# Optimization experiments

Hardware: AMD Instinct MI355X
Metric: run time of the kernel (lower is better)

The kernel has to match this reference:

```python
import jax, jax.numpy as jnp
import numpy as np

V, E, H, B, T, K = 50000, 100, 128, 128, 512, 12
HD = H // 2  # per-direction LSTM hidden = 64
START, STOP = 10, 11


def _lstm_params(k):
    k1, k2, k3, k4 = jax.random.split(k, 4)
    s = 1.0 / np.sqrt(HD)
    return (jax.random.uniform(k1, (4 * HD, E), minval=-s, maxval=s),
            jax.random.uniform(k2, (4 * HD, HD), minval=-s, maxval=s),
            jax.random.uniform(k3, (4 * HD,), minval=-s, maxval=s),
            jax.random.uniform(k4, (4 * HD,), minval=-s, maxval=s))


def setup_inputs() -> dict:
    key = jax.random.key(0)
    ks = jax.random.split(key, 10)
    sentences = jax.random.randint(ks[0], (B, T), 0, V)
    emb = jax.random.normal(ks[1], (V, E)) * 0.1
    Wih_f, Whh_f, bih_f, bhh_f = _lstm_params(ks[2])
    Wih_b, Whh_b, bih_b, bhh_b = _lstm_params(ks[3])
    W_out = jax.random.normal(ks[4], (K, H)) * 0.05
    b_out = jnp.zeros((K,), dtype=jnp.float32)
    transitions = jax.random.normal(ks[5], (K, K))
    transitions = transitions.at[:, START].set(-10000.0).at[STOP, :].set(-10000.0)
    h0 = jax.random.normal(ks[6], (2, B, HD))
    c0 = jax.random.normal(ks[7], (2, B, HD))
    return dict(sentences=sentences, emb=emb,
                Wih_f=Wih_f, Whh_f=Whh_f, bih_f=bih_f, bhh_f=bhh_f,
                Wih_b=Wih_b, Whh_b=Whh_b, bih_b=bih_b, bhh_b=bhh_b,
                W_out=W_out, b_out=b_out, transitions=transitions, h0=h0, c0=c0)


def _lstm_dir(x, h0, c0, Wih, Whh, bih, bhh):
    # x: [T,B,E]; PyTorch gate order i,f,g,o
    def step(carry, xt):
        h, c = carry
        g = xt @ Wih.T + h @ Whh.T + bih + bhh  # [B,4HD]
        i, f, gg, o = jnp.split(g, 4, axis=-1)
        c = jax.nn.sigmoid(f) * c + jax.nn.sigmoid(i) * jnp.tanh(gg)
        h = jax.nn.sigmoid(o) * jnp.tanh(c)
        return (h, c), h
    _, hs = jax.lax.scan(step, (h0, c0), x)
    return hs  # [T,B,HD]


def _viterbi(emis, trans):
    # emis: [T,K]
    def step(prev, em_t):
        v = prev[:, None] + trans          # [K_from, K_to]
        nxt = em_t + jnp.max(v, axis=0)
        return nxt, jnp.argmax(v, axis=0)  # backpointer per to-tag
    last, bps = jax.lax.scan(step, emis[0], emis[1:])  # bps: [T-1,K]
    last_tag = jnp.argmax(last)
    score = jnp.max(last)
    def back(tag, bp):
        prev = bp[tag]
        return prev, prev
    _, head = jax.lax.scan(back, last_tag, bps, reverse=True)  # tags[0..T-2]
    path = jnp.concatenate([head, last_tag[None]])
    return score, path


def reference(sentences, emb, Wih_f, Whh_f, bih_f, bhh_f,
              Wih_b, Whh_b, bih_b, bhh_b, W_out, b_out,
              transitions, h0, c0):
    x = emb[sentences]              # [B,T,E]
    xt = jnp.swapaxes(x, 0, 1)      # [T,B,E]
    hf = _lstm_dir(xt, h0[0], c0[0], Wih_f, Whh_f, bih_f, bhh_f)
    hb = _lstm_dir(xt[::-1], h0[1], c0[1], Wih_b, Whh_b, bih_b, bhh_b)[::-1]
    hcat = jnp.concatenate([hf, hb], axis=-1)      # [T,B,H]
    emis = hcat @ W_out.T + b_out                  # [T,B,K]
    emis = jnp.swapaxes(emis, 0, 1)                # [B,T,K]
    scores, paths = jax.vmap(lambda e: _viterbi(e, transitions))(emis)
    return scores, paths
```

## Files before the change

kernel.cpp:

```cpp
#include <hip/hip_runtime.h>
#include <hip/hip_bf16.h>

#define VV 50000
#define EE 100
#define HD 64
#define BB 128
#define TT 512
#define KK 12

typedef unsigned int  uint32;
typedef unsigned short ushort16;
typedef __bf16 bf16x8 __attribute__((ext_vector_type(8)));
typedef float  f32x4  __attribute__((ext_vector_type(4)));

__device__ __forceinline__ float bf_lo(unsigned u) { return __uint_as_float(u << 16); }
__device__ __forceinline__ float bf_hi(unsigned u) { return __uint_as_float(u & 0xffff0000u); }
__device__ __forceinline__ float rl_f(float v, int lane) {
    return __uint_as_float(__builtin_amdgcn_readlane(__float_as_uint(v), lane));
}
__device__ __forceinline__ float sigm_f(float x) { return 1.f / (1.f + __expf(-x)); }
__device__ __forceinline__ float tanh_f(float x) {
    float e = __expf(2.f * x);
    return 1.f - 2.f / (e + 1.f);
}
__device__ __forceinline__ unsigned short f2bf(float v) {
    return __builtin_bit_cast(unsigned short, __float2bfloat16(v));
}

#define LDK 136

__global__ __launch_bounds__(256) void k1_mfma(
    const float* __restrict__ emb,
    const float* __restrict__ Wih_f, const float* __restrict__ Wih_b,
    __hip_bfloat16* __restrict__ proj)
{
    __shared__ unsigned short lA[64 * LDK];
    __shared__ unsigned short lB[64 * LDK];

    const int tid = threadIdx.x;
    const int v0  = blockIdx.x * 64;
    const int jb  = blockIdx.y;
    const float* Wsrc = ((jb < 4) ? Wih_f : Wih_b) + (size_t)(jb & 3) * 64 * EE;

    for (int i = tid; i < 64 * 20; i += 256) {
        int r = i / 20, c2 = i % 20;
        int off = r * LDK + 96 + c2 * 2;
        *(uint32*)&lA[off] = 0u;
        *(uint32*)&lB[off] = 0u;
    }
    {
        const float* asrc = emb + (size_t)v0 * EE;
        const int alim = (VV - v0 < 64 ? VV - v0 : 64) * EE;
        for (int i = tid; i < 64 * EE; i += 256) {
            float v = (i < alim) ? asrc[i] : 0.f;
            lA[(i / EE) * LDK + (i % EE)] = f2bf(v);
        }
    }
    for (int i = tid; i < 64 * EE; i += 256) {
        lB[(i / EE) * LDK + (i % EE)] = f2bf(Wsrc[i]);
    }
    __syncthreads();

    const int w = tid >> 6, l = tid & 63;
    const int lo16 = l & 15, hi = l >> 4;

    f32x4 acc[4] = { {0.f,0.f,0.f,0.f}, {0.f,0.f,0.f,0.f},
                     {0.f,0.f,0.f,0.f}, {0.f,0.f,0.f,0.f} };
    #pragma unroll
    for (int s = 0; s < 4; ++s) {
        bf16x8 af = *(const bf16x8*)&lA[(w * 16 + lo16) * LDK + s * 32 + hi * 8];
        #pragma unroll
        for (int n = 0; n < 4; ++n) {
            bf16x8 bfr = *(const bf16x8*)&lB[(n * 16 + lo16) * LDK + s * 32 + hi * 8];
            acc[n] = __builtin_amdgcn_mfma_f32_16x16x32_bf16(af, bfr, acc[n], 0, 0, 0);
        }
    }
    #pragma unroll
    for (int n = 0; n < 4; ++n) {
        #pragma unroll
        for (int r = 0; r < 4; ++r) {
            int v = v0 + w * 16 + hi * 4 + r;
            int j = jb * 64 + n * 16 + lo16;
            if (v < VV)
                proj[(size_t)v * 512 + j] = __float2bfloat16(acc[n][r]);
        }
    }
}

__global__ __launch_bounds__(256) void k2_lstm(
    const int* __restrict__ sent,
    const __hip_bfloat16* __restrict__ proj,
    const float* __restrict__ Whh_f, const float* __restrict__ Whh_b,
    const float* __restrict__ bih_f, const float* __restrict__ bhh_f,
    const float* __restrict__ bih_b, const float* __restrict__ bhh_b,
    const float* __restrict__ h0, const float* __restrict__ c0,
    __hip_bfloat16* __restrict__ Hbuf)
{
    const int b   = blockIdx.x >> 1;
    const int d   = blockIdx.x & 1;
    const int tid = threadIdx.x;
    const int u   = tid & 63;
    const int w   = tid >> 6;

    __shared__ float a_lds[2][256];

    const float* Whh = (d == 0 ? Whh_f : Whh_b) + (size_t)tid * HD;
    float wreg[HD];
    #pragma unroll
    for (int k = 0; k < HD / 4; ++k) {
        float4 t = reinterpret_cast<const float4*>(Whh)[k];
        wreg[4*k+0] = t.x; wreg[4*k+1] = t.y; wreg[4*k+2] = t.z; wreg[4*k+3] = t.w;
    }
    const float bias = (d == 0) ? (bih_f[tid] + bhh_f[tid]) : (bih_b[tid] + bhh_b[tid]);

    float h = h0[((size_t)d * BB + b) * HD + u];
    float c = c0[((size_t)d * BB + b) * HD + u];

    const int* srow = sent + (size_t)b * TT;
    int t0 = (d == 0) ? 0 : TT - 1;
    int t1 = (d == 0) ? 1 : TT - 2;
    float xp0 = __bfloat162float(proj[(size_t)srow[t0] * 512 + d * 256 + tid]);
    float xp1 = __bfloat162float(proj[(size_t)srow[t1] * 512 + d * 256 + tid]);

    int pb = 0;
    for (int s = 0; s < TT; ++s) {
        const int t  = (d == 0) ? s : TT - 1 - s;
        const int sp = (s + 2 < TT) ? s + 2 : s;
        const int tp = (d == 0) ? sp : TT - 1 - sp;
        float xpn = __bfloat162float(proj[(size_t)srow[tp] * 512 + d * 256 + tid]);

        float acc0 = bias + xp0, acc1 = 0.f, acc2 = 0.f, acc3 = 0.f;
        #pragma unroll
        for (int k = 0; k < HD; k += 4) {
            float hk0 = rl_f(h, k + 0);
            float hk1 = rl_f(h, k + 1);
            float hk2 = rl_f(h, k + 2);
            float hk3 = rl_f(h, k + 3);
            acc0 = fmaf(hk0, wreg[k + 0], acc0);
            acc1 = fmaf(hk1, wreg[k + 1], acc1);
            acc2 = fmaf(hk2, wreg[k + 2], acc2);
            acc3 = fmaf(hk3, wreg[k + 3], acc3);
        }
        float g = (acc0 + acc1) + (acc2 + acc3);

        float a = (w == 2) ? tanh_f(g) : sigm_f(g);
        a_lds[pb][tid] = a;
        __syncthreads();
        float ai = a_lds[pb][u];
        float af = a_lds[pb][64 + u];
        float ag = a_lds[pb][128 + u];
        float ao = a_lds[pb][192 + u];
        c = af * c + ai * ag;
        h = ao * tanh_f(c);
        pb ^= 1;

        if (tid < 64)
            Hbuf[((size_t)t * BB + b) * 128 + d * 64 + u] = __float2bfloat16(h);

        xp0 = xp1; xp1 = xpn;
    }
}

__global__ __launch_bounds__(128) void k3_emis(
    const __hip_bfloat16* __restrict__ Hbuf,
    const float* __restrict__ W_out, const float* __restrict__ b_out,
    float* __restrict__ emis)
{
    const int t = blockIdx.x;
    const int b = threadIdx.x;
    __shared__ float Wl[KK * 128];
    for (int i = threadIdx.x; i < KK * 128; i += 128) Wl[i] = W_out[i];
    __syncthreads();

    const __hip_bfloat16* hrow = Hbuf + ((size_t)t * BB + b) * 128;
    float acc[KK];
    #pragma unroll
    for (int k = 0; k < KK; ++k) acc[k] = b_out[k];

    #pragma unroll
    for (int u0 = 0; u0 < 128; u0 += 8) {
        uint4 hv = *reinterpret_cast<const uint4*>(hrow + u0);
        float hf[8];
        hf[0] = bf_lo(hv.x); hf[1] = bf_hi(hv.x);
        hf[2] = bf_lo(hv.y); hf[3] = bf_hi(hv.y);
        hf[4] = bf_lo(hv.z); hf[5] = bf_hi(hv.z);
        hf[6] = bf_lo(hv.w); hf[7] = bf_hi(hv.w);
        #pragma unroll
        for (int k = 0; k < KK; ++k) {
            #pragma unroll
            for (int r = 0; r < 8; ++r)
                acc[k] = fmaf(hf[r], Wl[k * 128 + u0 + r], acc[k]);
        }
    }
    float* e = emis + ((size_t)b * TT + t) * KK;
    #pragma unroll
    for (int k = 0; k < KK; k += 4) {
        float4 v = make_float4(acc[k], acc[k+1], acc[k+2], acc[k+3]);
        *reinterpret_cast<float4*>(e + k) = v;
    }
}

__global__ __launch_bounds__(64) void k4_viterbi(
    const float* __restrict__ emis, const float* __restrict__ trans,
    float* __restrict__ out)
{
    const int b    = blockIdx.x;
    const int lane = threadIdx.x;
    __shared__ float em_lds[TT * KK];
    __shared__ unsigned char bp[(TT - 1) * KK + 4];

    {
        const uint4* e4 = reinterpret_cast<const uint4*>(emis + (size_t)b * TT * KK);
        uint4* l4 = reinterpret_cast<uint4*>(em_lds);
        for (int i = lane; i < TT * KK / 4; i += 64) l4[i] = e4[i];
    }
    __syncthreads();

    const int jj = (lane < KK) ? lane : 0;
    float tc[KK];
    #pragma unroll
    for (int i = 0; i < KK; ++i) tc[i] = trans[i * KK + jj];

    float vj = em_lds[jj];
    float sv[KK];
    #pragma unroll
    for (int i = 0; i < KK; ++i) sv[i] = rl_f(vj, i);

    for (int t = 1; t < TT; ++t) {
        float best = sv[0] + tc[0];
        int bi = 0;
        #pragma unroll
        for (int i = 1; i < KK; ++i) {
            float cnd = sv[i] + tc[i];
            bool gt = cnd > best;
            best = gt ? cnd : best;
            bi   = gt ? i : bi;
        }
        if (lane < KK) bp[(t - 1) * KK + lane] = (unsigned char)bi;
        vj = best + em_lds[t * KK + jj];
        #pragma unroll
        for (int i = 0; i < KK; ++i) sv[i] = rl_f(vj, i);
    }

    float best = sv[0]; int bt = 0;
    #pragma unroll
    for (int i = 1; i < KK; ++i) { if (sv[i] > best) { best = sv[i]; bt = i; } }

    if (lane == 0) {
        out[b] = best;
        float* path = out + BB + (size_t)b * TT;
        int tag = bt;
        path[TT - 1] = (float)tag;
        for (int t = TT - 2; t >= 0; --t) {
            tag = bp[t * KK + tag];
            path[t] = (float)tag;
        }
    }
}

extern "C" void kernel_launch(void* const* d_in, const int* in_sizes, int n_in,
                              void* d_out, int out_size, void* d_ws, size_t ws_size,
                              hipStream_t stream) {
    const int*   sent  = (const int*)  d_in[0];
    const float* emb   = (const float*)d_in[1];
    const float* Wih_f = (const float*)d_in[2];
    const float* Whh_f = (const float*)d_in[3];
    const float* bih_f = (const float*)d_in[4];
    const float* bhh_f = (const float*)d_in[5];
    const float* Wih_b = (const float*)d_in[6];
    const float* Whh_b = (const float*)d_in[7];
    const float* bih_b = (const float*)d_in[8];
    const float* bhh_b = (const float*)d_in[9];
    const float* W_out = (const float*)d_in[10];
    const float* b_out = (const float*)d_in[11];
    const float* trans = (const float*)d_in[12];
    const float* h0    = (const float*)d_in[13];
    const float* c0    = (const float*)d_in[14];
    float* out = (float*)d_out;

    char* ws = (char*)d_ws;
    __hip_bfloat16* proj = (__hip_bfloat16*)ws;
    size_t off = (((size_t)VV * 512 * 2) + 255) & ~(size_t)255;
    __hip_bfloat16* Hbuf = (__hip_bfloat16*)(ws + off);
    off += (((size_t)TT * BB * 128 * 2) + 255) & ~(size_t)255;
    float* emis = (float*)(ws + off);

    dim3 g1((VV + 63) / 64, 8);
    k1_mfma<<<g1, 256, 0, stream>>>(emb, Wih_f, Wih_b, proj);
    k2_lstm<<<dim3(2 * BB), 256, 0, stream>>>(sent, proj, Whh_f, Whh_b,
                                              bih_f, bhh_f, bih_b, bhh_b,
                                              h0, c0, Hbuf);
    k3_emis<<<dim3(TT), 128, 0, stream>>>(Hbuf, W_out, b_out, emis);
    k4_viterbi<<<dim3(BB), 64, 0, stream>>>(emis, trans, out);
}
```

Baseline: 639.0 us.

## Reuse embedding tile across all gate blocks in projection kernel; streamline LSTM loop

```diff
diff --git a/kernel.cpp b/kernel.cpp
--- a/kernel.cpp
+++ b/kernel.cpp
@@ -8,8 +8,7 @@
 #define TT 512
 #define KK 12
 
-typedef unsigned int  uint32;
-typedef unsigned short ushort16;
+typedef unsigned int uint32;
 typedef __bf16 bf16x8 __attribute__((ext_vector_type(8)));
 typedef float  f32x4  __attribute__((ext_vector_type(4)));
 
@@ -25,6 +24,11 @@
 }
 __device__ __forceinline__ unsigned short f2bf(float v) {
     return __builtin_bit_cast(unsigned short, __float2bfloat16(v));
+}
+__device__ __forceinline__ void lds_barrier() {
+    asm volatile("s_waitcnt lgkmcnt(0)" ::: "memory");
+    __builtin_amdgcn_s_barrier();
+    asm volatile("" ::: "memory");
 }
 
 #define LDK 136
@@ -39,14 +43,11 @@
 
     const int tid = threadIdx.x;
     const int v0  = blockIdx.x * 64;
-    const int jb  = blockIdx.y;
-    const float* Wsrc = ((jb < 4) ? Wih_f : Wih_b) + (size_t)(jb & 3) * 64 * EE;
 
     for (int i = tid; i < 64 * 20; i += 256) {
         int r = i / 20, c2 = i % 20;
-        int off = r * LDK + 96 + c2 * 2;
-        *(uint32*)&lA[off] = 0u;
-        *(uint32*)&lB[off] = 0u;
+        *(uint32*)&lA[r * LDK + 96 + c2 * 2] = 0u;
+        *(uint32*)&lB[r * LDK + 96 + c2 * 2] = 0u;
     }
     {
         const float* asrc = emb + (size_t)v0 * EE;
@@ -56,33 +57,42 @@
             lA[(i / EE) * LDK + (i % EE)] = f2bf(v);
         }
     }
-    for (int i = tid; i < 64 * EE; i += 256) {
-        lB[(i / EE) * LDK + (i % EE)] = f2bf(Wsrc[i]);
-    }
     __syncthreads();
 
     const int w = tid >> 6, l = tid & 63;
     const int lo16 = l & 15, hi = l >> 4;
 
-    f32x4 acc[4] = { {0.f,0.f,0.f,0.f}, {0.f,0.f,0.f,0.f},
-                     {0.f,0.f,0.f,0.f}, {0.f,0.f,0.f,0.f} };
-    #pragma unroll
-    for (int s = 0; s < 4; ++s) {
-        bf16x8 af = *(const bf16x8*)&lA[(w * 16 + lo16) * LDK + s * 32 + hi * 8];
+    bf16x8 afr[4];
+    #pragma unroll
+    for (int s = 0; s < 4; ++s)
+        afr[s] = *(const bf16x8*)&lA[(w * 16 + lo16) * LDK + s * 32 + hi * 8];
+
+    for (int jb = 0; jb < 8; ++jb) {
+        const float* Wsrc = ((jb < 4) ? Wih_f : Wih_b) + (size_t)(jb & 3) * 64 * EE;
+        __syncthreads();
+        for (int i = tid; i < 64 * EE; i += 256)
+            lB[(i / EE) * LDK + (i % EE)] = f2bf(Wsrc[i]);
+        __syncthreads();
+
+        f32x4 acc[4] = { {0.f,0.f,0.f,0.f}, {0.f,0.f,0.f,0.f},
+                         {0.f,0.f,0.f,0.f}, {0.f,0.f,0.f,0.f} };
+        #pragma unroll
+        for (int s = 0; s < 4; ++s) {
+            #pragma unroll
+            for (int n = 0; n < 4; ++n) {
+                bf16x8 bfr = *(const bf16x8*)&lB[(n * 16 + lo16) * LDK + s * 32 + hi * 8];
+                acc[n] = __builtin_amdgcn_mfma_f32_16x16x32_bf16(afr[s], bfr, acc[n], 0, 0, 0);
+            }
+        }
         #pragma unroll
         for (int n = 0; n < 4; ++n) {
-            bf16x8 bfr = *(const bf16x8*)&lB[(n * 16 + lo16) * LDK + s * 32 + hi * 8];
-            acc[n] = __builtin_amdgcn_mfma_f32_16x16x32_bf16(af, bfr, acc[n], 0, 0, 0);
-        }
-    }
-    #pragma unroll
-    for (int n = 0; n < 4; ++n) {
-        #pragma unroll
-        for (int r = 0; r < 4; ++r) {
-            int v = v0 + w * 16 + hi * 4 + r;
-            int j = jb * 64 + n * 16 + lo16;
-            if (v < VV)
-                proj[(size_t)v * 512 + j] = __float2bfloat16(acc[n][r]);
+            #pragma unroll
+            for (int r = 0; r < 4; ++r) {
+                int v = v0 + w * 16 + hi * 4 + r;
+                int j = jb * 64 + n * 16 + lo16;
+                if (v < VV)
+                    proj[(size_t)v * 512 + j] = __float2bfloat16(acc[n][r]);
+            }
         }
     }
 }
@@ -117,17 +127,21 @@
     float c = c0[((size_t)d * BB + b) * HD + u];
 
     const int* srow = sent + (size_t)b * TT;
-    int t0 = (d == 0) ? 0 : TT - 1;
-    int t1 = (d == 0) ? 1 : TT - 2;
+    const int tstep = (d == 0) ? 1 : -1;
+    const int t0    = (d == 0) ? 0 : TT - 1;
+
     float xp0 = __bfloat162float(proj[(size_t)srow[t0] * 512 + d * 256 + tid]);
-    float xp1 = __bfloat162float(proj[(size_t)srow[t1] * 512 + d * 256 + tid]);
+    float xp1 = __bfloat162float(proj[(size_t)srow[t0 + tstep] * 512 + d * 256 + tid]);
+    int  idx2 = srow[t0 + 2 * tstep];
+
+    __hip_bfloat16* hp = Hbuf + ((size_t)t0 * BB + b) * 128 + d * 64 + u;
+    const ptrdiff_t hstride = (ptrdiff_t)tstep * BB * 128;
 
     int pb = 0;
     for (int s = 0; s < TT; ++s) {
-        const int t  = (d == 0) ? s : TT - 1 - s;
-        const int sp = (s + 2 < TT) ? s + 2 : s;
-        const int tp = (d == 0) ? sp : TT - 1 - sp;
-        float xpn = __bfloat162float(proj[(size_t)srow[tp] * 512 + d * 256 + tid]);
+        float xpn = __bfloat162float(proj[(size_t)idx2 * 512 + d * 256 + tid]);
+        int s3 = (s + 3 < TT) ? s + 3 : TT - 1;
+        idx2 = srow[t0 + s3 * tstep];
 
         float acc0 = bias + xp0, acc1 = 0.f, acc2 = 0.f, acc3 = 0.f;
         #pragma unroll
@@ -145,7 +159,7 @@
 
         float a = (w == 2) ? tanh_f(g) : sigm_f(g);
         a_lds[pb][tid] = a;
-        __syncthreads();
+        lds_barrier();
         float ai = a_lds[pb][u];
         float af = a_lds[pb][64 + u];
         float ag = a_lds[pb][128 + u];
@@ -154,9 +168,10 @@
         h = ao * tanh_f(c);
         pb ^= 1;
 
-        if (tid < 64)
-            Hbuf[((size_t)t * BB + b) * 128 + d * 64 + u] = __float2bfloat16(h);
-
+        if (tid < 64) {
+            *hp = __float2bfloat16(h);
+            hp += hstride;
+        }
         xp0 = xp1; xp1 = xpn;
     }
 }
@@ -285,8 +300,7 @@
     off += (((size_t)TT * BB * 128 * 2) + 255) & ~(size_t)255;
     float* emis = (float*)(ws + off);
 
-    dim3 g1((VV + 63) / 64, 8);
-    k1_mfma<<<g1, 256, 0, stream>>>(emb, Wih_f, Wih_b, proj);
+    k1_mfma<<<dim3((VV + 63) / 64), 256, 0, stream>>>(emb, Wih_f, Wih_b, proj);
     k2_lstm<<<dim3(2 * BB), 256, 0, stream>>>(sent, proj, Whh_f, Whh_b,
                                               bih_f, bhh_f, bih_b, bhh_b,
                                               h0, c0, Hbuf);
```

After: 594.5 us. 1.07x faster.
